# Optimization experiments

Hardware: AMD Instinct MI355X
Metric: run time of the kernel (lower is better)

## Reference

```python
import jax, jax.numpy as jnp
import numpy as np

N, E, F_IN, H, ED = 8192, 524288, 39, 80, 4
MSG = 2 * H + ED          # 164, per-edge message dim
POST_IN = 12 * MSG        # 4 aggregators * 3 scalers
A_UMAP, B_UMAP = 0.583, 1.334


def setup_inputs() -> dict:
    key = jax.random.key(0)
    ks = jax.random.split(key, 16)
    s = 0.05
    return {
        "x": jax.random.normal(ks[0], (N, F_IN), jnp.float32),
        "edge_attr": jax.random.normal(ks[1], (E, ED), jnp.float32),
        "W_emb": jax.random.normal(ks[2], (F_IN, H), jnp.float32) * s,
        "b_emb": jnp.zeros((H,), jnp.float32),
        "W_post": jax.random.normal(ks[3], (4, POST_IN, H), jnp.float32) * s,
        "b_post": jnp.zeros((4, H), jnp.float32),
        "bn_gamma": jnp.ones((4, H), jnp.float32),
        "bn_beta": jnp.zeros((4, H), jnp.float32),
        "W1": jax.random.normal(ks[4], (H, 40), jnp.float32) * s,
        "b1": jnp.zeros((40,), jnp.float32),
        "W2": jax.random.normal(ks[5], (40, 20), jnp.float32) * s,
        "b2": jnp.zeros((20,), jnp.float32),
        "W3": jax.random.normal(ks[6], (20, 32), jnp.float32) * s,
        "b3": jnp.zeros((32,), jnp.float32),
        "edge_index": jax.random.randint(ks[7], (2, E), 0, N, jnp.int64),
        "batch": jnp.zeros((N,), jnp.int64),
    }


def reference(x, edge_attr, W_emb, b_emb, W_post, b_post, bn_gamma, bn_beta,
              W1, b1, W2, b2, W3, b3, edge_index, batch):
    src, dst = edge_index[0], edge_index[1]
    # degree-based scaler constants (PNA: amplification / attenuation)
    deg = jax.ops.segment_sum(jnp.ones((E,), x.dtype), dst, num_segments=N)
    logd = jnp.log1p(deg)
    avg_log = jnp.mean(logd)
    amp = (logd / avg_log)[:, None]
    att = jnp.where(logd > 0, avg_log / jnp.where(logd > 0, logd, 1.0), 1.0)[:, None]
    has = (deg > 0)[:, None]
    deg_safe = jnp.where(deg > 0, deg, 1.0)[:, None]

    h = x @ W_emb + b_emb                                  # [N, 80]
    for l in range(4):
        msg = jnp.concatenate([h[dst], h[src], edge_attr], axis=-1)  # [E, MSG]
        ssum = jax.ops.segment_sum(msg, dst, num_segments=N)
        mean = ssum / deg_safe
        ssq = jax.ops.segment_sum(msg * msg, dst, num_segments=N)
        std = jnp.sqrt(jax.nn.relu(ssq / deg_safe - mean * mean) + 1e-5)
        mn = jnp.where(has, jax.ops.segment_min(msg, dst, num_segments=N), 0.0)
        mx = jnp.where(has, jax.ops.segment_max(msg, dst, num_segments=N), 0.0)
        agg = jnp.concatenate([mean, mn, mx, std], axis=-1)           # [N, 4*MSG]
        out = jnp.concatenate([agg, agg * amp, agg * att], axis=-1)   # [N, POST_IN]
        out = out @ W_post[l] + b_post[l]                             # post_nn (1 layer)
        mu = out.mean(axis=0)
        var = out.var(axis=0)
        xhat = (out - mu) / jnp.sqrt(var + 1e-5)                      # BatchNorm
        h = jax.nn.relu(bn_gamma[l] * xhat + bn_beta[l]) + h          # relu + residual

    y = jax.nn.relu(h @ W1 + b1)
    y = jax.nn.relu(y @ W2 + b2)
    y = y @ W3 + b3                                       # [N, 32]
    # prob_low_dim: UMAP low-dim similarity 1/(1 + a * d^(2b))
    sq = jnp.sum(y * y, axis=-1)
    d2 = jnp.maximum(sq[:, None] + sq[None, :] - 2.0 * (y @ y.T), 0.0)
    return 1.0 / (1.0 + A_UMAP * d2 ** B_UMAP)            # [N, N]
```

## Files before the change

### kernel.cpp

```cpp
#include <hip/hip_runtime.h>
#include <hip/hip_bf16.h>
#include <math.h>

#define N_NODES 8192
#define N_EDGES 524288
#define HDIM 80
#define EDIM 4
#define MSG 164
#define K3 656
#define KP 672
#define A_UMAP 0.583f
#define B_UMAP 1.334f

typedef __attribute__((ext_vector_type(8))) short short8;
typedef __attribute__((ext_vector_type(4))) float f32x4;

__global__ __launch_bounds__(256) void deg_kernel(const int* __restrict__ ei,
                                                  int* __restrict__ deg) {
    int e = blockIdx.x * 256 + threadIdx.x;
    if (e < N_EDGES) atomicAdd(&deg[ei[N_EDGES + e]], 1);
}

__global__ __launch_bounds__(1024) void scan_kernel(const int* __restrict__ deg,
        int* __restrict__ offs, int* __restrict__ cursor,
        float* __restrict__ amp, float* __restrict__ att) {
    __shared__ int sdata[1024];
    __shared__ float sred[1024];
    int t = threadIdx.x;
    int loc[8];
    int s = 0;
    float ls = 0.f;
#pragma unroll
    for (int i = 0; i < 8; ++i) {
        int d = deg[t * 8 + i];
        loc[i] = d; s += d;
        ls += log1pf((float)d);
    }
    sdata[t] = s;
    sred[t] = ls;
    __syncthreads();
    for (int d = 1; d < 1024; d <<= 1) {
        int v = (t >= d) ? sdata[t - d] : 0;
        __syncthreads();
        sdata[t] += v;
        __syncthreads();
    }
    for (int d = 512; d > 0; d >>= 1) {
        if (t < d) sred[t] += sred[t + d];
        __syncthreads();
    }
    float avg = sred[0] / 8192.0f;
    int base = sdata[t] - s;
#pragma unroll
    for (int i = 0; i < 8; ++i) {
        int n = t * 8 + i;
        offs[n] = base;
        cursor[n] = base;
        base += loc[i];
        float ld = log1pf((float)loc[i]);
        amp[n] = ld / avg;
        att[n] = (loc[i] > 0) ? (avg / ld) : 1.0f;
    }
    if (t == 1023) offs[N_NODES] = base;
}

__global__ __launch_bounds__(256) void csr_fill(const int* __restrict__ ei,
        const float* __restrict__ edge_attr, int* __restrict__ cursor,
        int* __restrict__ csr_src, float* __restrict__ csr_ea) {
    int e = blockIdx.x * 256 + threadIdx.x;
    if (e >= N_EDGES) return;
    int src = ei[e];
    int dst = ei[N_EDGES + e];
    int pos = atomicAdd(&cursor[dst], 1);
    csr_src[pos] = src;
    float4 v = *(const float4*)(edge_attr + (size_t)e * 4);
    *(float4*)(csr_ea + (size_t)pos * 4) = v;
}

__global__ __launch_bounds__(256) void emb_kernel(const float* __restrict__ x,
        const float* __restrict__ W_emb, const float* __restrict__ b_emb,
        float* __restrict__ h) {
    __shared__ float Ws[39 * 80];
    __shared__ float xs[16][39];
    int t = threadIdx.x;
    int n0 = blockIdx.x * 16;
    for (int i = t; i < 39 * 80; i += 256) Ws[i] = W_emb[i];
    for (int i = t; i < 16 * 39; i += 256) xs[i / 39][i % 39] = x[(size_t)n0 * 39 + i];
    __syncthreads();
#pragma unroll
    for (int p = 0; p < 5; ++p) {
        int o = t + p * 256;
        int nl = o / 80, c = o % 80;
        float acc = b_emb[c];
#pragma unroll
        for (int f = 0; f < 39; ++f) acc = fmaf(xs[nl][f], Ws[f * 80 + c], acc);
        h[(size_t)(n0 + nl) * 80 + c] = acc;
    }
}

__global__ __launch_bounds__(256) void wconv(const float* __restrict__ W_post,
        __hip_bfloat16* __restrict__ WbT) {
    int idx = blockIdx.x * 256 + threadIdx.x;
    if (idx >= 4 * 3 * 80 * KP) return;
    int k = idx % KP;
    int rem = idx / KP;
    int c = rem % 80;
    int sl = rem / 80;
    float v = 0.f;
    if (k < K3) {
        int l = sl / 3, s = sl % 3;
        v = W_post[((size_t)l * 1968 + s * K3 + k) * 80 + c];
    }
    WbT[idx] = __float2bfloat16(v);
}

__global__ __launch_bounds__(128) void agg_kernel(const float* __restrict__ h,
        const int* __restrict__ offs, const int* __restrict__ csr_src,
        const float* __restrict__ csr_ea, __hip_bfloat16* __restrict__ aggb) {
    int w = threadIdx.x >> 6, l = threadIdx.x & 63;
    int n = blockIdx.x * 2 + w;
    int beg = offs[n], end = offs[n + 1];
    int deg = end - beg;
    bool has1h = (l < 16);
    bool has1e = (l >= 16 && l < 20);
    float s0 = 0.f, q0 = 0.f, mn0 = INFINITY, mx0 = -INFINITY;
    float s1 = 0.f, q1 = 0.f, mn1 = INFINITY, mx1 = -INFINITY;
    int i = beg;
    for (; i + 1 < end; i += 2) {
        int sA = csr_src[i], sB = csr_src[i + 1];
        float a0 = h[(size_t)sA * 80 + l];
        float b0 = h[(size_t)sB * 80 + l];
        float a1 = 0.f, b1 = 0.f;
        if (has1h) {
            a1 = h[(size_t)sA * 80 + 64 + l];
            b1 = h[(size_t)sB * 80 + 64 + l];
        } else if (has1e) {
            a1 = csr_ea[(size_t)i * 4 + (l - 16)];
            b1 = csr_ea[(size_t)(i + 1) * 4 + (l - 16)];
        }
        s0 += a0 + b0;
        q0 = fmaf(a0, a0, q0); q0 = fmaf(b0, b0, q0);
        mn0 = fminf(mn0, fminf(a0, b0)); mx0 = fmaxf(mx0, fmaxf(a0, b0));
        s1 += a1 + b1;
        q1 = fmaf(a1, a1, q1); q1 = fmaf(b1, b1, q1);
        mn1 = fminf(mn1, fminf(a1, b1)); mx1 = fmaxf(mx1, fmaxf(a1, b1));
    }
    if (i < end) {
        int sA = csr_src[i];
        float a0 = h[(size_t)sA * 80 + l];
        float a1 = 0.f;
        if (has1h) a1 = h[(size_t)sA * 80 + 64 + l];
        else if (has1e) a1 = csr_ea[(size_t)i * 4 + (l - 16)];
        s0 += a0; q0 = fmaf(a0, a0, q0);
        mn0 = fminf(mn0, a0); mx0 = fmaxf(mx0, a0);
        s1 += a1; q1 = fmaf(a1, a1, q1);
        mn1 = fminf(mn1, a1); mx1 = fmaxf(mx1, a1);
    }
    bool has = deg > 0;
    float invd = has ? (1.0f / (float)deg) : 1.0f;
    const float sd0 = 3.16227766e-3f;
    __hip_bfloat16* base = aggb + (size_t)n * KP;
    {
        float mean = s0 * invd;
        float var = fmaxf(q0 * invd - mean * mean, 0.f);
        float sd = sqrtf(var + 1e-5f);
        base[80 + l]       = __float2bfloat16(mean);
        base[164 + 80 + l] = __float2bfloat16(has ? mn0 : 0.f);
        base[328 + 80 + l] = __float2bfloat16(has ? mx0 : 0.f);
        base[492 + 80 + l] = __float2bfloat16(sd);
    }
    if (has1h) {
        float mean = s1 * invd;
        float var = fmaxf(q1 * invd - mean * mean, 0.f);
        float sd = sqrtf(var + 1e-5f);
        base[144 + l]       = __float2bfloat16(mean);
        base[164 + 144 + l] = __float2bfloat16(has ? mn1 : 0.f);
        base[328 + 144 + l] = __float2bfloat16(has ? mx1 : 0.f);
        base[492 + 144 + l] = __float2bfloat16(sd);
    } else if (has1e) {
        int d = l - 16;
        float mean = s1 * invd;
        float var = fmaxf(q1 * invd - mean * mean, 0.f);
        float sd = sqrtf(var + 1e-5f);
        base[160 + d]       = __float2bfloat16(mean);
        base[164 + 160 + d] = __float2bfloat16(has ? mn1 : 0.f);
        base[328 + 160 + d] = __float2bfloat16(has ? mx1 : 0.f);
        base[492 + 160 + d] = __float2bfloat16(sd);
    }
    {
        float hd = h[(size_t)n * 80 + l];
        float vd = has ? hd : 0.f;
        __hip_bfloat16 bv = __float2bfloat16(vd);
        base[l] = bv; base[164 + l] = bv; base[328 + l] = bv;
        base[492 + l] = __float2bfloat16(sd0);
    }
    if (l < 16) {
        float hd = h[(size_t)n * 80 + 64 + l];
        float vd = has ? hd : 0.f;
        __hip_bfloat16 bv = __float2bfloat16(vd);
        base[64 + l] = bv; base[164 + 64 + l] = bv; base[328 + 64 + l] = bv;
        base[492 + 64 + l] = __float2bfloat16(sd0);
        base[656 + l] = __float2bfloat16(0.f);
    }
}

__global__ __launch_bounds__(256) void post_gemm_mfma(
        const __hip_bfloat16* __restrict__ aggb,
        const __hip_bfloat16* __restrict__ WbT,
        float* __restrict__ G) {
    int s = blockIdx.y;
    int wave = threadIdx.x >> 6, lane = threadIdx.x & 63;
    int r0 = blockIdx.x * 64 + wave * 16;
    int lrow = lane & 15, koff = (lane >> 4) * 8;
    const __hip_bfloat16* Ap = aggb + (size_t)(r0 + lrow) * KP + koff;
    const __hip_bfloat16* Bp = WbT + ((size_t)s * 80 + lrow) * KP + koff;
    f32x4 acc[5] = {};
    for (int ks = 0; ks < KP / 32; ++ks) {
        short8 a = *(const short8*)(Ap + ks * 32);
#pragma unroll
        for (int c = 0; c < 5; ++c) {
            short8 b = *(const short8*)(Bp + (size_t)c * 16 * KP + ks * 32);
            acc[c] = __builtin_amdgcn_mfma_f32_16x16x32_bf16(a, b, acc[c], 0, 0, 0);
        }
    }
    int crow = (lane >> 4) * 4;
#pragma unroll
    for (int c = 0; c < 5; ++c)
#pragma unroll
        for (int r = 0; r < 4; ++r)
            G[((size_t)s * N_NODES + r0 + crow + r) * 80 + c * 16 + lrow] = acc[c][r];
}

__global__ __launch_bounds__(320) void combine_stats(const float* __restrict__ G,
        const float* __restrict__ amp, const float* __restrict__ att,
        const float* __restrict__ b_post_l, float* __restrict__ outb,
        float* __restrict__ stats) {
    const size_t NH = (size_t)N_NODES * 80;
    int t = threadIdx.x;
    int c = t % 80, rl = t / 80;
    int row0 = blockIdx.x * 64;
    float bc = b_post_l[c];
    float ssum = 0.f, ssq = 0.f;
    __shared__ float red[4][80], red2[4][80];
#pragma unroll
    for (int p = 0; p < 16; ++p) {
        int n = row0 + p * 4 + rl;
        size_t idx = (size_t)n * 80 + c;
        float v = G[idx] + amp[n] * G[NH + idx] + att[n] * G[2 * NH + idx] + bc;
        outb[idx] = v;
        ssum += v;
        ssq = fmaf(v, v, ssq);
    }
    red[rl][c] = ssum; red2[rl][c] = ssq;
    __syncthreads();
    if (rl == 0) {
        float a = red[0][c] + red[1][c] + red[2][c] + red[3][c];
        float b = red2[0][c] + red2[1][c] + red2[2][c] + red2[3][c];
        atomicAdd(&stats[c], a);
        atomicAdd(&stats[80 + c], b);
    }
}

__global__ __launch_bounds__(256) void bn_apply(const float* __restrict__ outb,
        const float* __restrict__ stats, const float* __restrict__ gamma,
        const float* __restrict__ beta, float* __restrict__ h) {
    size_t idx = (size_t)blockIdx.x * 256 + threadIdx.x;
    int c = (int)(idx % 80);
    float mu = stats[c] * (1.0f / 8192.0f);
    float var = stats[80 + c] * (1.0f / 8192.0f) - mu * mu;
    float xh = (outb[idx] - mu) * rsqrtf(var + 1e-5f);
    h[idx] += fmaxf(fmaf(gamma[c], xh, beta[c]), 0.f);
}

__global__ __launch_bounds__(256) void mlp_kernel(const float* __restrict__ h,
        const float* __restrict__ W1, const float* __restrict__ b1,
        const float* __restrict__ W2, const float* __restrict__ b2,
        const float* __restrict__ W3, const float* __restrict__ b3,
        __hip_bfloat16* __restrict__ yb, float* __restrict__ sq) {
    __shared__ float W1s[3200], W2s[800], W3s[640];
    __shared__ float b1s[40], b2s[20], b3s[32];
    __shared__ float hs[32][80], x1s[32][40], x2s[32][20], ys[32][33];
    int t = threadIdx.x;
    int n0 = blockIdx.x * 32;
    for (int i = t; i < 3200; i += 256) W1s[i] = W1[i];
    for (int i = t; i < 800; i += 256) W2s[i] = W2[i];
    for (int i = t; i < 640; i += 256) W3s[i] = W3[i];
    if (t < 40) b1s[t] = b1[t];
    else if (t < 60) b2s[t - 40] = b2[t - 40];
    else if (t < 92) b3s[t - 60] = b3[t - 60];
    for (int i = t; i < 2560; i += 256) hs[i / 80][i % 80] = h[(size_t)n0 * 80 + i];
    __syncthreads();
#pragma unroll
    for (int p = 0; p < 5; ++p) {
        int o = t + p * 256;
        int nl = o / 40, j = o % 40;
        float acc = b1s[j];
#pragma unroll
        for (int f = 0; f < 80; ++f) acc = fmaf(hs[nl][f], W1s[f * 40 + j], acc);
        x1s[nl][j] = fmaxf(acc, 0.f);
    }
    __syncthreads();
    for (int o = t; o < 640; o += 256) {
        int nl = o / 20, j = o % 20;
        float acc = b2s[j];
#pragma unroll
        for (int f = 0; f < 40; ++f) acc = fmaf(x1s[nl][f], W2s[f * 20 + j], acc);
        x2s[nl][j] = fmaxf(acc, 0.f);
    }
    __syncthreads();
#pragma unroll
    for (int p = 0; p < 4; ++p) {
        int o = t + p * 256;
        int nl = o / 32, c = o % 32;
        float acc = b3s[c];
#pragma unroll
        for (int f = 0; f < 20; ++f) acc = fmaf(x2s[nl][f], W3s[f * 32 + c], acc);
        __hip_bfloat16 bv = __float2bfloat16(acc);
        yb[(size_t)(n0 + nl) * 32 + c] = bv;
        ys[nl][c] = __bfloat162float(bv);
    }
    __syncthreads();
    if (t < 32) {
        float s = 0.f;
#pragma unroll
        for (int c = 0; c < 32; ++c) s = fmaf(ys[t][c], ys[t][c], s);
        sq[n0 + t] = s;
    }
}

__global__ __launch_bounds__(256) void pairwise_mfma(
        const __hip_bfloat16* __restrict__ yb,
        const float* __restrict__ sq, float* __restrict__ out) {
    int t = threadIdx.x;
    int wave = t >> 6, lane = t & 63;
    int i0 = blockIdx.y * 128 + wave * 32;
    int j0 = blockIdx.x * 128;
    int lrow = lane & 15, koff = (lane >> 4) * 8;
    short8 a0 = *(const short8*)(yb + (size_t)(i0 + lrow) * 32 + koff);
    short8 a1 = *(const short8*)(yb + (size_t)(i0 + 16 + lrow) * 32 + koff);
    f32x4 z = {0.f, 0.f, 0.f, 0.f};
    f32x4 acc[2][8];
#pragma unroll
    for (int f = 0; f < 8; ++f) {
        short8 b = *(const short8*)(yb + (size_t)(j0 + f * 16 + lrow) * 32 + koff);
        acc[0][f] = __builtin_amdgcn_mfma_f32_16x16x32_bf16(a0, b, z, 0, 0, 0);
        acc[1][f] = __builtin_amdgcn_mfma_f32_16x16x32_bf16(a1, b, z, 0, 0, 0);
    }
    float sj[8];
#pragma unroll
    for (int f = 0; f < 8; ++f) sj[f] = sq[j0 + f * 16 + lrow];
    int crow = (lane >> 4) * 4;
#pragma unroll
    for (int hh = 0; hh < 2; ++hh) {
#pragma unroll
        for (int r = 0; r < 4; ++r) {
            int irow = i0 + hh * 16 + crow + r;
            float si = sq[irow];
            size_t rowbase = (size_t)irow * N_NODES + j0 + lrow;
#pragma unroll
            for (int f = 0; f < 8; ++f) {
                float d2 = fmaxf(si + sj[f] - 2.0f * acc[hh][f][r], 0.f);
                float u = exp2f(B_UMAP * log2f(d2));
                out[rowbase + f * 16] = 1.0f / fmaf(A_UMAP, u, 1.0f);
            }
        }
    }
}

extern "C" void kernel_launch(void* const* d_in, const int* in_sizes, int n_in,
                              void* d_out, int out_size, void* d_ws, size_t ws_size,
                              hipStream_t stream) {
    const float* x         = (const float*)d_in[0];
    const float* edge_attr = (const float*)d_in[1];
    const float* W_emb     = (const float*)d_in[2];
    const float* b_emb     = (const float*)d_in[3];
    const float* W_post    = (const float*)d_in[4];
    const float* b_post    = (const float*)d_in[5];
    const float* bn_gamma  = (const float*)d_in[6];
    const float* bn_beta   = (const float*)d_in[7];
    const float* W1        = (const float*)d_in[8];
    const float* b1        = (const float*)d_in[9];
    const float* W2        = (const float*)d_in[10];
    const float* b2        = (const float*)d_in[11];
    const float* W3        = (const float*)d_in[12];
    const float* b3        = (const float*)d_in[13];
    const int*   ei        = (const int*)d_in[14];
    float* out = (float*)d_out;

    char* p = (char*)d_ws;
    auto alloc = [&](size_t b) { char* r = p; p += (b + 255) & ~(size_t)255; return r; };
    int*   deg     = (int*)alloc((size_t)N_NODES * 4);
    float* stats4  = (float*)alloc((size_t)4 * 160 * 4);
    int*   offs    = (int*)alloc((size_t)(N_NODES + 1) * 4);
    int*   cursor  = (int*)alloc((size_t)N_NODES * 4);
    float* amp     = (float*)alloc((size_t)N_NODES * 4);
    float* att     = (float*)alloc((size_t)N_NODES * 4);
    int*   csr_src = (int*)alloc((size_t)N_EDGES * 4);
    float* csr_ea  = (float*)alloc((size_t)N_EDGES * 16);
    float* h       = (float*)alloc((size_t)N_NODES * 80 * 4);
    __hip_bfloat16* aggb = (__hip_bfloat16*)alloc((size_t)N_NODES * KP * 2);
    __hip_bfloat16* WbT  = (__hip_bfloat16*)alloc((size_t)4 * 3 * 80 * KP * 2);
    float* G       = (float*)alloc((size_t)3 * N_NODES * 80 * 4);
    float* outb    = (float*)alloc((size_t)N_NODES * 80 * 4);
    __hip_bfloat16* yb = (__hip_bfloat16*)alloc((size_t)N_NODES * 32 * 2);
    float* sq      = (float*)alloc((size_t)N_NODES * 4);

    (void)hipMemsetAsync(deg, 0, (size_t)N_NODES * 4 + 4 * 160 * 4, stream);
    deg_kernel<<<N_EDGES / 256, 256, 0, stream>>>(ei, deg);
    scan_kernel<<<1, 1024, 0, stream>>>(deg, offs, cursor, amp, att);
    csr_fill<<<N_EDGES / 256, 256, 0, stream>>>(ei, edge_attr, cursor, csr_src, csr_ea);
    emb_kernel<<<N_NODES / 16, 256, 0, stream>>>(x, W_emb, b_emb, h);
    wconv<<<(4 * 3 * 80 * KP + 255) / 256, 256, 0, stream>>>(W_post, WbT);

    for (int l = 0; l < 4; ++l) {
        agg_kernel<<<N_NODES / 2, 128, 0, stream>>>(h, offs, csr_src, csr_ea, aggb);
        post_gemm_mfma<<<dim3(N_NODES / 64, 3), 256, 0, stream>>>(
            aggb, WbT + (size_t)l * 3 * 80 * KP, G);
        combine_stats<<<N_NODES / 64, 320, 0, stream>>>(
            G, amp, att, b_post + l * 80, outb, stats4 + l * 160);
        bn_apply<<<(N_NODES * 80) / 256, 256, 0, stream>>>(
            outb, stats4 + l * 160, bn_gamma + l * 80, bn_beta + l * 80, h);
    }

    mlp_kernel<<<N_NODES / 32, 256, 0, stream>>>(h, W1, b1, W2, b2, W3, b3, yb, sq);
    pairwise_mfma<<<dim3(N_NODES / 128, N_NODES / 128), 256, 0, stream>>>(yb, sq, out);
}
```

Before: 668.9 us.

## Fuse post GEMM with scaler combine and BN stats; merge embed and weight-convert kernels

The three-scaler post GEMM now runs in one kernel that computes all three scaler partials per row tile. It applies amp/att and bias in registers, writes outb directly, and reduces the BatchNorm column sums with shuffles and shared atomics. This removes the intermediate G buffer round trip and one launch per layer. The embedding and weight-conversion kernels are merged into one launch, and the pairwise output division is replaced with a hardware reciprocal. The cost is a larger accumulator footprint (15 MFMA tiles per wave), a grid of 128-thread blocks, and slightly less precise reciprocals.

```diff
diff --git a/kernel.cpp b/kernel.cpp
--- a/kernel.cpp
+++ b/kernel.cpp
@@ -77,41 +77,41 @@
     *(float4*)(csr_ea + (size_t)pos * 4) = v;
 }
 
-__global__ __launch_bounds__(256) void emb_kernel(const float* __restrict__ x,
+__global__ __launch_bounds__(256) void emb_wconv(const float* __restrict__ x,
         const float* __restrict__ W_emb, const float* __restrict__ b_emb,
-        float* __restrict__ h) {
-    __shared__ float Ws[39 * 80];
-    __shared__ float xs[16][39];
+        float* __restrict__ h, const float* __restrict__ W_post,
+        __hip_bfloat16* __restrict__ WbT) {
     int t = threadIdx.x;
-    int n0 = blockIdx.x * 16;
-    for (int i = t; i < 39 * 80; i += 256) Ws[i] = W_emb[i];
-    for (int i = t; i < 16 * 39; i += 256) xs[i / 39][i % 39] = x[(size_t)n0 * 39 + i];
-    __syncthreads();
-#pragma unroll
-    for (int p = 0; p < 5; ++p) {
-        int o = t + p * 256;
-        int nl = o / 80, c = o % 80;
-        float acc = b_emb[c];
-#pragma unroll
-        for (int f = 0; f < 39; ++f) acc = fmaf(xs[nl][f], Ws[f * 80 + c], acc);
-        h[(size_t)(n0 + nl) * 80 + c] = acc;
-    }
-}
-
-__global__ __launch_bounds__(256) void wconv(const float* __restrict__ W_post,
-        __hip_bfloat16* __restrict__ WbT) {
-    int idx = blockIdx.x * 256 + threadIdx.x;
-    if (idx >= 4 * 3 * 80 * KP) return;
-    int k = idx % KP;
-    int rem = idx / KP;
-    int c = rem % 80;
-    int sl = rem / 80;
-    float v = 0.f;
-    if (k < K3) {
-        int l = sl / 3, s = sl % 3;
-        v = W_post[((size_t)l * 1968 + s * K3 + k) * 80 + c];
-    }
-    WbT[idx] = __float2bfloat16(v);
+    if (blockIdx.x < 512) {
+        __shared__ float Ws[39 * 80];
+        __shared__ float xs[16][39];
+        int n0 = blockIdx.x * 16;
+        for (int i = t; i < 39 * 80; i += 256) Ws[i] = W_emb[i];
+        for (int i = t; i < 16 * 39; i += 256) xs[i / 39][i % 39] = x[(size_t)n0 * 39 + i];
+        __syncthreads();
+#pragma unroll
+        for (int p = 0; p < 5; ++p) {
+            int o = t + p * 256;
+            int nl = o / 80, c = o % 80;
+            float acc = b_emb[c];
+#pragma unroll
+            for (int f = 0; f < 39; ++f) acc = fmaf(xs[nl][f], Ws[f * 80 + c], acc);
+            h[(size_t)(n0 + nl) * 80 + c] = acc;
+        }
+    } else {
+        int idx = (blockIdx.x - 512) * 256 + t;
+        if (idx >= 4 * 3 * 80 * KP) return;
+        int k = idx % KP;
+        int rem = idx / KP;
+        int c = rem % 80;
+        int sl = rem / 80;
+        float v = 0.f;
+        if (k < K3) {
+            int l = sl / 3, s = sl % 3;
+            v = W_post[((size_t)l * 1968 + s * K3 + k) * 80 + c];
+        }
+        WbT[idx] = __float2bfloat16(v);
+    }
 }
 
 __global__ __launch_bounds__(128) void agg_kernel(const float* __restrict__ h,
@@ -204,61 +204,65 @@
     }
 }
 
-__global__ __launch_bounds__(256) void post_gemm_mfma(
+__global__ __launch_bounds__(128) void gemm_combine(
         const __hip_bfloat16* __restrict__ aggb,
         const __hip_bfloat16* __restrict__ WbT,
-        float* __restrict__ G) {
-    int s = blockIdx.y;
-    int wave = threadIdx.x >> 6, lane = threadIdx.x & 63;
-    int r0 = blockIdx.x * 64 + wave * 16;
+        const float* __restrict__ amp, const float* __restrict__ att,
+        const float* __restrict__ b_post_l,
+        float* __restrict__ outb, float* __restrict__ stats) {
+    __shared__ float sred[160];
+    int t = threadIdx.x;
+    for (int i = t; i < 160; i += 128) sred[i] = 0.f;
+    int wave = t >> 6, lane = t & 63;
+    int r0 = blockIdx.x * 32 + wave * 16;
     int lrow = lane & 15, koff = (lane >> 4) * 8;
     const __hip_bfloat16* Ap = aggb + (size_t)(r0 + lrow) * KP + koff;
-    const __hip_bfloat16* Bp = WbT + ((size_t)s * 80 + lrow) * KP + koff;
-    f32x4 acc[5] = {};
+    const __hip_bfloat16* Bp = WbT + (size_t)lrow * KP + koff;
+    f32x4 acc[3][5] = {};
     for (int ks = 0; ks < KP / 32; ++ks) {
         short8 a = *(const short8*)(Ap + ks * 32);
 #pragma unroll
+        for (int s = 0; s < 3; ++s)
+#pragma unroll
+            for (int c = 0; c < 5; ++c) {
+                short8 b = *(const short8*)(Bp + ((size_t)s * 80 + c * 16) * KP + ks * 32);
+                acc[s][c] = __builtin_amdgcn_mfma_f32_16x16x32_bf16(a, b, acc[s][c], 0, 0, 0);
+            }
+    }
+    __syncthreads();
+    int crow = (lane >> 4) * 4;
+    float bc[5];
+#pragma unroll
+    for (int c = 0; c < 5; ++c) bc[c] = b_post_l[c * 16 + lrow];
+    float colsum[5] = {}, colsq[5] = {};
+#pragma unroll
+    for (int r = 0; r < 4; ++r) {
+        int row = r0 + crow + r;
+        float am = amp[row], at = att[row];
+#pragma unroll
         for (int c = 0; c < 5; ++c) {
-            short8 b = *(const short8*)(Bp + (size_t)c * 16 * KP + ks * 32);
-            acc[c] = __builtin_amdgcn_mfma_f32_16x16x32_bf16(a, b, acc[c], 0, 0, 0);
-        }
-    }
-    int crow = (lane >> 4) * 4;
-#pragma unroll
-    for (int c = 0; c < 5; ++c)
-#pragma unroll
-        for (int r = 0; r < 4; ++r)
-            G[((size_t)s * N_NODES + r0 + crow + r) * 80 + c * 16 + lrow] = acc[c][r];
-}
-
-__global__ __launch_bounds__(320) void combine_stats(const float* __restrict__ G,
-        const float* __restrict__ amp, const float* __restrict__ att,
-        const float* __restrict__ b_post_l, float* __restrict__ outb,
-        float* __restrict__ stats) {
-    const size_t NH = (size_t)N_NODES * 80;
-    int t = threadIdx.x;
-    int c = t % 80, rl = t / 80;
-    int row0 = blockIdx.x * 64;
-    float bc = b_post_l[c];
-    float ssum = 0.f, ssq = 0.f;
-    __shared__ float red[4][80], red2[4][80];
-#pragma unroll
-    for (int p = 0; p < 16; ++p) {
-        int n = row0 + p * 4 + rl;
-        size_t idx = (size_t)n * 80 + c;
-        float v = G[idx] + amp[n] * G[NH + idx] + att[n] * G[2 * NH + idx] + bc;
-        outb[idx] = v;
-        ssum += v;
-        ssq = fmaf(v, v, ssq);
-    }
-    red[rl][c] = ssum; red2[rl][c] = ssq;
-    __syncthreads();
-    if (rl == 0) {
-        float a = red[0][c] + red[1][c] + red[2][c] + red[3][c];
-        float b = red2[0][c] + red2[1][c] + red2[2][c] + red2[3][c];
-        atomicAdd(&stats[c], a);
-        atomicAdd(&stats[80 + c], b);
-    }
+            float v = acc[0][c][r] + am * acc[1][c][r] + at * acc[2][c][r] + bc[c];
+            outb[(size_t)row * 80 + c * 16 + lrow] = v;
+            colsum[c] += v;
+            colsq[c] = fmaf(v, v, colsq[c]);
+        }
+    }
+#pragma unroll
+    for (int c = 0; c < 5; ++c) {
+        colsum[c] += __shfl_xor(colsum[c], 16);
+        colsum[c] += __shfl_xor(colsum[c], 32);
+        colsq[c]  += __shfl_xor(colsq[c], 16);
+        colsq[c]  += __shfl_xor(colsq[c], 32);
+    }
+    if ((lane >> 4) == 0) {
+#pragma unroll
+        for (int c = 0; c < 5; ++c) {
+            atomicAdd(&sred[c * 16 + lrow], colsum[c]);
+            atomicAdd(&sred[80 + c * 16 + lrow], colsq[c]);
+        }
+    }
+    __syncthreads();
+    for (int i = t; i < 160; i += 128) atomicAdd(&stats[i], sred[i]);
 }
 
 __global__ __launch_bounds__(256) void bn_apply(const float* __restrict__ outb,
@@ -361,7 +365,7 @@
             for (int f = 0; f < 8; ++f) {
                 float d2 = fmaxf(si + sj[f] - 2.0f * acc[hh][f][r], 0.f);
                 float u = exp2f(B_UMAP * log2f(d2));
-                out[rowbase + f * 16] = 1.0f / fmaf(A_UMAP, u, 1.0f);
+                out[rowbase + f * 16] = __builtin_amdgcn_rcpf(fmaf(A_UMAP, u, 1.0f));
             }
         }
     }
@@ -400,7 +404,6 @@
     float* h       = (float*)alloc((size_t)N_NODES * 80 * 4);
     __hip_bfloat16* aggb = (__hip_bfloat16*)alloc((size_t)N_NODES * KP * 2);
     __hip_bfloat16* WbT  = (__hip_bfloat16*)alloc((size_t)4 * 3 * 80 * KP * 2);
-    float* G       = (float*)alloc((size_t)3 * N_NODES * 80 * 4);
     float* outb    = (float*)alloc((size_t)N_NODES * 80 * 4);
     __hip_bfloat16* yb = (__hip_bfloat16*)alloc((size_t)N_NODES * 32 * 2);
     float* sq      = (float*)alloc((size_t)N_NODES * 4);
@@ -409,15 +412,14 @@
     deg_kernel<<<N_EDGES / 256, 256, 0, stream>>>(ei, deg);
     scan_kernel<<<1, 1024, 0, stream>>>(deg, offs, cursor, amp, att);
     csr_fill<<<N_EDGES / 256, 256, 0, stream>>>(ei, edge_attr, cursor, csr_src, csr_ea);
-    emb_kernel<<<N_NODES / 16, 256, 0, stream>>>(x, W_emb, b_emb, h);
-    wconv<<<(4 * 3 * 80 * KP + 255) / 256, 256, 0, stream>>>(W_post, WbT);
+    emb_wconv<<<512 + (4 * 3 * 80 * KP + 255) / 256, 256, 0, stream>>>(
+        x, W_emb, b_emb, h, W_post, WbT);
 
     for (int l = 0; l < 4; ++l) {
         agg_kernel<<<N_NODES / 2, 128, 0, stream>>>(h, offs, csr_src, csr_ea, aggb);
-        post_gemm_mfma<<<dim3(N_NODES / 64, 3), 256, 0, stream>>>(
-            aggb, WbT + (size_t)l * 3 * 80 * KP, G);
-        combine_stats<<<N_NODES / 64, 320, 0, stream>>>(
-            G, amp, att, b_post + l * 80, outb, stats4 + l * 160);
+        gemm_combine<<<N_NODES / 32, 128, 0, stream>>>(
+            aggb, WbT + (size_t)l * 3 * 80 * KP, amp, att, b_post + l * 80,
+            outb, stats4 + l * 160);
         bn_apply<<<(N_NODES * 80) / 256, 256, 0, stream>>>(
             outb, stats4 + l * 160, bn_gamma + l * 80, bn_beta + l * 80, h);
     }
```

Result: faster. 651.3 us (-2.6%).
